# Performance work log

Measured on AMD Instinct MI355X. Metric: run time of the kernel, lower is better.

Reference implementation:

```python
import jax, jax.numpy as jnp
import numpy as np

EPS = 1e-12
CLAMP = 1.0 - 1e-6


def _hamilton(a, b):
    r1, i1, j1, k1 = a
    r2, i2, j2, k2 = b
    return (r1 * r2 - i1 * i2 - j1 * j2 - k1 * k2,
            r1 * i2 + i1 * r2 + j1 * k2 - k1 * j2,
            r1 * j2 - i1 * k2 + j1 * r2 + k1 * i2,
            r1 * k2 + i1 * j2 - j1 * i2 + k1 * r2)


def _chained_prod(r, i, j, k):
    """Left-to-right Hamilton product along the last axis via tree reduction."""
    n = r.shape[-1]
    m = 1 << (n - 1).bit_length()  # next power of two
    if m != n:
        pad = [(0, 0)] * (r.ndim - 1) + [(0, m - n)]
        # pad with identity quaternion (1,0,0,0)
        r = jnp.pad(r, pad, constant_values=1.0)
        i = jnp.pad(i, pad)
        j = jnp.pad(j, pad)
        k = jnp.pad(k, pad)
    q = (r, i, j, k)
    while q[0].shape[-1] > 1:
        a = tuple(t[..., 0::2] for t in q)
        b = tuple(t[..., 1::2] for t in q)
        q = _hamilton(a, b)
    return tuple(t[..., 0] for t in q)


def reference(x, weight, bias):
    # x: (B, T, 4*C_in) laid out as [r | i | j | k]; weight: (C_out, C_in); bias: (C_out,)
    r, i, j, k = jnp.split(x, 4, axis=-1)  # each (B, T, C_in)
    norm_v = jnp.sqrt(i * i + j * j + k * k + EPS)
    theta = jnp.arccos(jnp.clip(r, -CLAMP, CLAMP))  # (B, T, C_in)
    # quaternion power: angle scaled by weight, shifted by bias -> (B, T, C_out, C_in)
    theta = weight * theta[..., None, :] + bias[:, None]
    mul = jnp.sin(theta) / norm_v[..., None, :]
    qr = jnp.cos(theta)
    qi = i[..., None, :] * mul
    qj = j[..., None, :] * mul
    qk = k[..., None, :] * mul
    # chained Hamilton product over C_in -> (B, T, C_out)
    pr, pi, pj, pk = _chained_prod(qr, qi, qj, qk)
    # quaternion normalize
    n = jnp.sqrt(pr * pr + pi * pi + pj * pj + pk * pk + EPS)
    return jnp.concatenate([pr / n, pi / n, pj / n, pk / n], axis=-1)  # (B, T, 4*C_out)


def setup_inputs() -> dict:
    key = jax.random.key(0)
    k1, k2, k3 = jax.random.split(key, 3)
    C_in, C_out = 64, 128
    x = jax.random.normal(k1, (16, 128, 4 * C_in), dtype=jnp.float32)
    a = float(np.sqrt(6.0 / (C_in + C_out)))  # xavier bound
    weight = jax.random.uniform(k2, (C_out, C_in), minval=-a, maxval=a, dtype=jnp.float32)
    bias = jax.random.uniform(k3, (C_out,), minval=-a, maxval=a, dtype=jnp.float32)
    return {"x": x, "weight": weight, "bias": bias}
```

## Files before the change

### kernel.cpp

```cpp
#include <hip/hip_runtime.h>
#include <math.h>


typedef float v2f __attribute__((ext_vector_type(2)));

#define C_IN   64
#define C_OUT  128
#define POS_PER_BLOCK 4
#define BLOCK  (POS_PER_BLOCK * 64)
#define WSTR2  (C_OUT / 2 + 1)

#define INV_2PI 0.15915494309189535f

__global__ __launch_bounds__(BLOCK, 2) void qpu_kernel(
    const float* __restrict__ x,
    const float* __restrict__ weight,
    const float* __restrict__ bias,
    float* __restrict__ out,
    int P)
{
    __shared__ float  w_s[C_IN * WSTR2 * 2];
    __shared__ float4 pre[POS_PER_BLOCK][C_IN];

    const int tid  = threadIdx.x;
    const int lane = tid & 63;
    const int sub  = tid >> 6;

    {
        const float4* w4 = (const float4*)weight;
        #pragma unroll
        for (int idx = tid; idx < (C_OUT * C_IN) / 4; idx += BLOCK) {
            const float4 v = w4[idx];
            const int o  = idx >> 4;
            const int c0 = (idx & 15) * 4;
            w_s[(c0 + 0) * (2 * WSTR2) + o] = v.x;
            w_s[(c0 + 1) * (2 * WSTR2) + o] = v.y;
            w_s[(c0 + 2) * (2 * WSTR2) + o] = v.z;
            w_s[(c0 + 3) * (2 * WSTR2) + o] = v.w;
        }
    }

    const int pos = blockIdx.x * POS_PER_BLOCK + sub;
    const bool valid = (pos < P);

    if (valid) {
        const int c = lane;
        const float* xb = x + (size_t)pos * (4 * C_IN);
        const float r = xb[c];
        const float i = xb[C_IN + c];
        const float j = xb[2 * C_IN + c];
        const float k = xb[3 * C_IN + c];
        const float rc = fminf(fmaxf(r, -0.999999f), 0.999999f);
        const float th0 = acosf(rc);
        const float inv = rsqrtf(fmaf(i, i, fmaf(j, j, fmaf(k, k, 1e-12f))));
        pre[sub][c] = make_float4(th0, i * inv, j * inv, k * inv);
    }
    __syncthreads();

    if (!valid) return;

    const v2f b2 = ((const v2f*)bias)[lane] * INV_2PI;
    const v2f* __restrict__ w2 = (const v2f*)w_s;

    v2f pr = 1.0f, pi = 0.0f, pj = 0.0f, pk = 0.0f;

    #pragma unroll 8
    for (int c = 0; c < C_IN; ++c) {
        const float4 p4 = pre[sub][c];
        const v2f    w  = w2[c * WSTR2 + lane];
        const float  thr = p4.x * INV_2PI;
        const v2f    rev = w * thr + b2;
        v2f s, ct;
        s.x  = __builtin_amdgcn_sinf(rev.x);
        s.y  = __builtin_amdgcn_sinf(rev.y);
        ct.x = __builtin_amdgcn_cosf(rev.x);
        ct.y = __builtin_amdgcn_cosf(rev.y);
        const v2f qi = p4.y * s;
        const v2f qj = p4.z * s;
        const v2f qk = p4.w * s;
        const v2f nr = pr * ct - pi * qi - pj * qj - pk * qk;
        const v2f ni = pr * qi + pi * ct + pj * qk - pk * qj;
        const v2f nj = pr * qj - pi * qk + pj * ct + pk * qi;
        const v2f nk = pr * qk + pi * qj - pj * qi + pk * ct;
        pr = nr; pi = ni; pj = nj; pk = nk;
    }

    const v2f n2 = pr * pr + pi * pi + pj * pj + pk * pk + 1e-12f;
    v2f invn;
    invn.x = rsqrtf(n2.x);
    invn.y = rsqrtf(n2.y);
    pr *= invn; pi *= invn; pj *= invn; pk *= invn;

    float* ob = out + (size_t)pos * (4 * C_OUT);
    ((v2f*)(ob              ))[lane] = pr;
    ((v2f*)(ob +     C_OUT  ))[lane] = pi;
    ((v2f*)(ob + 2 * C_OUT  ))[lane] = pj;
    ((v2f*)(ob + 3 * C_OUT  ))[lane] = pk;
}

extern "C" void kernel_launch(void* const* d_in, const int* in_sizes, int n_in,
                              void* d_out, int out_size, void* d_ws, size_t ws_size,
                              hipStream_t stream) {
    const float* x      = (const float*)d_in[0];
    const float* weight = (const float*)d_in[1];
    const float* bias   = (const float*)d_in[2];
    float* out          = (float*)d_out;

    const int P = in_sizes[0] / (4 * C_IN);
    const int grid = (P + POS_PER_BLOCK - 1) / POS_PER_BLOCK;

    qpu_kernel<<<grid, BLOCK, 0, stream>>>(x, weight, bias, out, P);
}
```

Before: 67.40 us.

## Split C_in chain across two waves and combine partial quaternion products

Each position is now handled by two waves, each computing the Hamilton product over half of the input channels. The second half's partial product is passed through shared memory and multiplied into the first half's result before normalization. This halves the serial dependency chain per wave and doubles the block size, which may help latency hiding. The cost is an extra barrier, more shared memory, and idle waves during the preprocessing and combine phases. With launch bounds fixed at 2 blocks of 512 threads, register pressure and occupancy may shift.

```diff
diff --git a/kernel.cpp b/kernel.cpp
--- a/kernel.cpp
+++ b/kernel.cpp
@@ -7,7 +7,8 @@
 #define C_IN   64
 #define C_OUT  128
 #define POS_PER_BLOCK 4
-#define BLOCK  (POS_PER_BLOCK * 64)
+#define BLOCK  512
+#define HALF   (C_IN / 2)
 #define WSTR2  (C_OUT / 2 + 1)
 
 #define INV_2PI 0.15915494309189535f
@@ -21,10 +22,13 @@
 {
     __shared__ float  w_s[C_IN * WSTR2 * 2];
     __shared__ float4 pre[POS_PER_BLOCK][C_IN];
+    __shared__ v2f    part[POS_PER_BLOCK][4][64];
 
     const int tid  = threadIdx.x;
     const int lane = tid & 63;
-    const int sub  = tid >> 6;
+    const int wave = tid >> 6;
+    const int sub  = wave >> 1;
+    const int half = wave & 1;
 
     {
         const float4* w4 = (const float4*)weight;
@@ -43,59 +47,81 @@
     const int pos = blockIdx.x * POS_PER_BLOCK + sub;
     const bool valid = (pos < P);
 
-    if (valid) {
-        const int c = lane;
-        const float* xb = x + (size_t)pos * (4 * C_IN);
-        const float r = xb[c];
-        const float i = xb[C_IN + c];
-        const float j = xb[2 * C_IN + c];
-        const float k = xb[3 * C_IN + c];
-        const float rc = fminf(fmaxf(r, -0.999999f), 0.999999f);
-        const float th0 = acosf(rc);
-        const float inv = rsqrtf(fmaf(i, i, fmaf(j, j, fmaf(k, k, 1e-12f))));
-        pre[sub][c] = make_float4(th0, i * inv, j * inv, k * inv);
+    {
+        const int t = tid & 127;
+        if (valid && t < C_IN) {
+            const int c = t;
+            const float* xb = x + (size_t)pos * (4 * C_IN);
+            const float r = xb[c];
+            const float i = xb[C_IN + c];
+            const float j = xb[2 * C_IN + c];
+            const float k = xb[3 * C_IN + c];
+            const float rc = fminf(fmaxf(r, -0.999999f), 0.999999f);
+            const float th0 = acosf(rc);
+            const float inv = rsqrtf(fmaf(i, i, fmaf(j, j, fmaf(k, k, 1e-12f))));
+            pre[sub][c] = make_float4(th0, i * inv, j * inv, k * inv);
+        }
     }
     __syncthreads();
-
-    if (!valid) return;
 
     const v2f b2 = ((const v2f*)bias)[lane] * INV_2PI;
     const v2f* __restrict__ w2 = (const v2f*)w_s;
 
     v2f pr = 1.0f, pi = 0.0f, pj = 0.0f, pk = 0.0f;
 
-    #pragma unroll 8
-    for (int c = 0; c < C_IN; ++c) {
-        const float4 p4 = pre[sub][c];
-        const v2f    w  = w2[c * WSTR2 + lane];
-        const float  thr = p4.x * INV_2PI;
-        const v2f    rev = w * thr + b2;
-        v2f s, ct;
-        s.x  = __builtin_amdgcn_sinf(rev.x);
-        s.y  = __builtin_amdgcn_sinf(rev.y);
-        ct.x = __builtin_amdgcn_cosf(rev.x);
-        ct.y = __builtin_amdgcn_cosf(rev.y);
-        const v2f qi = p4.y * s;
-        const v2f qj = p4.z * s;
-        const v2f qk = p4.w * s;
-        const v2f nr = pr * ct - pi * qi - pj * qj - pk * qk;
-        const v2f ni = pr * qi + pi * ct + pj * qk - pk * qj;
-        const v2f nj = pr * qj - pi * qk + pj * ct + pk * qi;
-        const v2f nk = pr * qk + pi * qj - pj * qi + pk * ct;
-        pr = nr; pi = ni; pj = nj; pk = nk;
+    if (valid) {
+        const int c0 = half * HALF;
+        #pragma unroll 8
+        for (int cc = 0; cc < HALF; ++cc) {
+            const int c = c0 + cc;
+            const float4 p4 = pre[sub][c];
+            const v2f    w  = w2[c * WSTR2 + lane];
+            const v2f    rev = w * (p4.x * INV_2PI) + b2;
+            v2f s, ct;
+            s.x  = __builtin_amdgcn_sinf(rev.x);
+            s.y  = __builtin_amdgcn_sinf(rev.y);
+            ct.x = __builtin_amdgcn_cosf(rev.x);
+            ct.y = __builtin_amdgcn_cosf(rev.y);
+            const v2f qi = p4.y * s;
+            const v2f qj = p4.z * s;
+            const v2f qk = p4.w * s;
+            const v2f nr = pr * ct - pi * qi - pj * qj - pk * qk;
+            const v2f ni = pr * qi + pi * ct + pj * qk - pk * qj;
+            const v2f nj = pr * qj - pi * qk + pj * ct + pk * qi;
+            const v2f nk = pr * qk + pi * qj - pj * qi + pk * ct;
+            pr = nr; pi = ni; pj = nj; pk = nk;
+        }
     }
 
-    const v2f n2 = pr * pr + pi * pi + pj * pj + pk * pk + 1e-12f;
+    if (half == 1) {
+        part[sub][0][lane] = pr;
+        part[sub][1][lane] = pi;
+        part[sub][2][lane] = pj;
+        part[sub][3][lane] = pk;
+    }
+    __syncthreads();
+
+    if (!valid || half == 1) return;
+
+    const v2f Br = part[sub][0][lane];
+    const v2f Bi = part[sub][1][lane];
+    const v2f Bj = part[sub][2][lane];
+    const v2f Bk = part[sub][3][lane];
+    const v2f tr = pr * Br - pi * Bi - pj * Bj - pk * Bk;
+    const v2f ti = pr * Bi + pi * Br + pj * Bk - pk * Bj;
+    const v2f tj = pr * Bj - pi * Bk + pj * Br + pk * Bi;
+    const v2f tk = pr * Bk + pi * Bj - pj * Bi + pk * Br;
+
+    const v2f n2 = tr * tr + ti * ti + tj * tj + tk * tk + 1e-12f;
     v2f invn;
     invn.x = rsqrtf(n2.x);
     invn.y = rsqrtf(n2.y);
-    pr *= invn; pi *= invn; pj *= invn; pk *= invn;
 
     float* ob = out + (size_t)pos * (4 * C_OUT);
-    ((v2f*)(ob              ))[lane] = pr;
-    ((v2f*)(ob +     C_OUT  ))[lane] = pi;
-    ((v2f*)(ob + 2 * C_OUT  ))[lane] = pj;
-    ((v2f*)(ob + 3 * C_OUT  ))[lane] = pk;
+    ((v2f*)(ob            ))[lane] = tr * invn;
+    ((v2f*)(ob +     C_OUT))[lane] = ti * invn;
+    ((v2f*)(ob + 2 * C_OUT))[lane] = tj * invn;
+    ((v2f*)(ob + 3 * C_OUT))[lane] = tk * invn;
 }
 
 extern "C" void kernel_launch(void* const* d_in, const int* in_sizes, int n_in,
```

Result: no change. 67.25 us (-0.2%).
